# Kernel tuning notes

Hardware: AMD Instinct MI355X
Metric: run time of the kernel (lower is better)

Reference implementation:

```python
import jax, jax.numpy as jnp
import numpy as np

DESC_DIM = 128


def setup_inputs() -> dict:
    key = jax.random.key(0)
    # [B=1, desc_dim+1, H, W] dense Unet output: 128 descriptor channels + 1 heatmap channel
    features = jax.random.normal(key, (1, DESC_DIM + 1, 1024, 1024), dtype=jnp.float32)
    return {
        "features": features,
        "orig_w": 1024,
        "orig_h": 1024,
        "max_keypoints": 2048,
        "window": 5,
    }


def reference(features, orig_w, orig_h, max_keypoints, window):
    # DISK.detect + DISK.compute (inference path):
    # max-pool NMS on heatmap, keep positives inside original image bounds,
    # take top max_keypoints by score, gather + L2-normalize descriptors.
    D = features.shape[1] - 1
    heatmap = features[0, D]            # [H, W]
    desc = features[0, :D]              # [D, H, W]
    H, W = heatmap.shape

    # local-max NMS: equality with 5x5 max pool (ties measure-zero for float data)
    pooled = jax.lax.reduce_window(
        heatmap, -jnp.inf, jax.lax.max,
        window_dimensions=(window, window), window_strides=(1, 1), padding="SAME")
    ys = jnp.arange(H)[:, None]
    xs = jnp.arange(W)[None, :]
    in_bounds = (xs <= orig_w - 1) & (ys <= orig_h - 1)  # 'valid' filter in detect()
    mask = (heatmap == pooled) & (heatmap > 0.0) & in_bounds  # cutoff=0.0

    # replace nonzero + kthvalue + argsort with masked top-k (jit-friendly, same math)
    flat = jnp.where(mask, heatmap, -jnp.inf).reshape(-1)  # [H*W]
    scores, idx = jax.lax.top_k(flat, max_keypoints)       # [K], [K]
    y = idx // W
    x = idx % W
    keypoints = jnp.stack([x, y], axis=-1).astype(jnp.float32)  # [K, 2] (x, y)

    d = desc.reshape(D, -1)[:, idx].T                      # [K, D] gather
    d = d / jnp.maximum(jnp.linalg.norm(d, axis=-1, keepdims=True), 1e-12)  # F.normalize

    valid = jnp.isfinite(scores)  # padding indicator when fewer than K detections
    return keypoints, scores, d, valid
```

## Files before the change

kernel.cpp:

```cpp
#include <hip/hip_runtime.h>
#include <stdint.h>
#include <math.h>

#define WIDTH  1024
#define HEIGHT 1024
#define DDIM   128
#define TOPK   2048
#define CAP    131072
#define SELCAP 4096

#define HIST_OFF 64
#define KEYS_OFF (HIST_OFF + 65536 * 4)
#define SEL_OFF  (KEYS_OFF + CAP * 8)
#define SIDX_OFF (SEL_OFF + SELCAP * 8)

__global__ __launch_bounds__(1024) void find_candidates(
        const float* __restrict__ feat,
        const int* __restrict__ p_ow, const int* __restrict__ p_oh,
        unsigned int* __restrict__ hdr,
        unsigned int* __restrict__ hist,
        unsigned long long* __restrict__ keys) {
    const int x = threadIdx.x;
    const int y = blockIdx.x;
    const float* hm = feat + (size_t)DDIM * WIDTH * HEIGHT;

    __shared__ unsigned long long lkeys[256];
    __shared__ unsigned int lcnt, lbase;
    if (x == 0) lcnt = 0u;
    __syncthreads();

    float c = hm[y * WIDTH + x];
    if ((c > 0.0f) && (x <= p_ow[0] - 1) && (y <= p_oh[0] - 1)) {
        int xm2 = max(x - 2, 0), xm1 = max(x - 1, 0);
        int xp1 = min(x + 1, WIDTH - 1), xp2 = min(x + 2, WIDTH - 1);
        int ym2 = max(y - 2, 0), ym1 = max(y - 1, 0);
        int yp1 = min(y + 1, HEIGHT - 1), yp2 = min(y + 2, HEIGHT - 1);
        const float* r0 = hm + ym1 * WIDTH;
        const float* r1 = hm + y   * WIDTH;
        const float* r2 = hm + yp1 * WIDTH;
        float m = fmaxf(fmaxf(fmaxf(r0[xm1], r0[x]), fmaxf(r0[xp1], r1[xm1])),
                        fmaxf(fmaxf(r1[xp1], r2[xm1]), fmaxf(r2[x], r2[xp1])));
        if (m <= c) {
            const float* ra = hm + ym2 * WIDTH;
            const float* rb = hm + yp2 * WIDTH;
            float m2 = fmaxf(fmaxf(fmaxf(ra[xm2], ra[xm1]), fmaxf(ra[x], ra[xp1])), ra[xp2]);
            m2 = fmaxf(m2, fmaxf(fmaxf(rb[xm2], rb[xm1]), fmaxf(fmaxf(rb[x], rb[xp1]), rb[xp2])));
            m2 = fmaxf(m2, fmaxf(fmaxf(r0[xm2], r0[xp2]), fmaxf(r1[xm2], r1[xp2])));
            m2 = fmaxf(m2, fmaxf(r2[xm2], r2[xp2]));
            if (m2 <= c) {
                unsigned int idx = (unsigned int)(y * WIDTH + x);
                unsigned long long key =
                    ((unsigned long long)__float_as_uint(c) << 32) |
                    (unsigned long long)(~idx);
                unsigned int p = atomicAdd(&lcnt, 1u);
                if (p < 256u) lkeys[p] = key;
            }
        }
    }
    __syncthreads();
    if (x == 0) lbase = atomicAdd(&hdr[0], lcnt);
    __syncthreads();
    unsigned int n = lcnt < 256u ? lcnt : 256u;
    unsigned int base = lbase;
    for (unsigned int i = x; i < n; i += blockDim.x) {
        unsigned long long k = lkeys[i];
        if (base + i < CAP) keys[base + i] = k;
        atomicAdd(&hist[(unsigned int)(k >> 48)], 1u);
    }
}

__global__ __launch_bounds__(1024) void scan_hist(
        unsigned int* __restrict__ hdr,
        const unsigned int* __restrict__ hist) {
    __shared__ unsigned int part[1024];
    const int tid = threadIdx.x;
    const unsigned int base = (unsigned int)tid * 64u;
    unsigned int s = 0;
    #pragma unroll 8
    for (int j = 0; j < 64; ++j) s += hist[base + j];
    part[tid] = s;
    __syncthreads();
    for (int d = 1; d < 1024; d <<= 1) {
        unsigned int v = (tid + d < 1024) ? part[tid + d] : 0u;
        __syncthreads();
        part[tid] += v;
        __syncthreads();
    }
    unsigned int N = hdr[0]; if (N > CAP) N = CAP;
    unsigned int target = N < TOPK ? N : TOPK;
    if (tid == 0) { hdr[3] = target; if (target == 0) hdr[2] = 0u; }
    if (target == 0) return;
    unsigned int St = part[tid];
    unsigned int Sn = (tid < 1023) ? part[tid + 1] : 0u;
    if (St >= target && Sn < target) {
        unsigned int above = Sn;
        unsigned int B = base;
        for (int b = (int)base + 63; b >= (int)base; --b) {
            unsigned int h = hist[b];
            if (above + h >= target) { B = (unsigned int)b; break; }
            above += h;
        }
        hdr[2] = B;
    }
}

__global__ void filter_keys(unsigned int* __restrict__ hdr,
                            const unsigned long long* __restrict__ keys,
                            unsigned long long* __restrict__ sel) {
    unsigned int N = hdr[0]; if (N > CAP) N = CAP;
    unsigned long long B = (unsigned long long)hdr[2];
    unsigned int stride = gridDim.x * blockDim.x;
    for (unsigned int i = blockIdx.x * blockDim.x + threadIdx.x; i < N; i += stride) {
        unsigned long long k = keys[i];
        if ((k >> 48) >= B) {
            unsigned int p = atomicAdd(&hdr[1], 1u);
            if (p < SELCAP) sel[p] = k;
        }
    }
}

__global__ __launch_bounds__(1024) void sort_emit(
        const unsigned int* __restrict__ hdr,
        const unsigned long long* __restrict__ sel,
        float* __restrict__ out_kp, float* __restrict__ out_sc,
        float* __restrict__ out_vd, unsigned int* __restrict__ sidx) {
    __shared__ unsigned long long sk[SELCAP];
    const int tid = threadIdx.x;
    unsigned int M = hdr[1]; if (M > SELCAP) M = SELCAP;
    unsigned int KK = hdr[3];
    for (unsigned int i = tid; i < SELCAP; i += 1024) sk[i] = (i < M) ? sel[i] : 0ull;
    __syncthreads();
    for (unsigned int size = 2; size <= SELCAP; size <<= 1) {
        for (unsigned int str = size >> 1; str > 0; str >>= 1) {
            for (unsigned int i = tid; i < SELCAP; i += 1024) {
                unsigned int j = i ^ str;
                if (j > i) {
                    unsigned long long a = sk[i], b = sk[j];
                    bool desc = ((i & size) == 0);
                    if (desc ? (a < b) : (a > b)) { sk[i] = b; sk[j] = a; }
                }
            }
            __syncthreads();
        }
    }
    for (unsigned int r = tid; r < TOPK; r += 1024) {
        unsigned long long k = sk[r];
        bool live = (r < KK);
        unsigned int idx = ~(unsigned int)(k & 0xFFFFFFFFull);
        out_kp[2 * r + 0] = live ? (float)(idx & (WIDTH - 1)) : 0.0f;
        out_kp[2 * r + 1] = live ? (float)(idx >> 10) : 0.0f;
        out_sc[r] = live ? __uint_as_float((unsigned int)(k >> 32)) : -INFINITY;
        out_vd[r] = live ? 1.0f : 0.0f;
        sidx[r]   = live ? idx : 0u;
    }
}

__global__ __launch_bounds__(128) void gather_desc(
        const float* __restrict__ feat,
        const unsigned int* __restrict__ sidx,
        float* __restrict__ out_d) {
    int kp = blockIdx.x;
    int c  = threadIdx.x;
    unsigned int idx = sidx[kp];
    float v = feat[(size_t)c * (WIDTH * HEIGHT) + idx];
    float s = v * v;
    #pragma unroll
    for (int off = 32; off > 0; off >>= 1) s += __shfl_down(s, off, 64);
    __shared__ float sw[2];
    if ((c & 63) == 0) sw[c >> 6] = s;
    __syncthreads();
    float norm = fmaxf(sqrtf(sw[0] + sw[1]), 1e-12f);
    out_d[(size_t)kp * DDIM + c] = v / norm;
}

extern "C" void kernel_launch(void* const* d_in, const int* in_sizes, int n_in,
                              void* d_out, int out_size, void* d_ws, size_t ws_size,
                              hipStream_t stream) {
    const float* feat = (const float*)d_in[0];
    const int* p_ow = (const int*)d_in[1];
    const int* p_oh = (const int*)d_in[2];

    float* out = (float*)d_out;
    float* out_kp = out;
    float* out_sc = out + 2 * TOPK;
    float* out_d  = out + 3 * TOPK;
    float* out_vd = out + 3 * TOPK + TOPK * DDIM;

    unsigned int* hdr  = (unsigned int*)d_ws;
    unsigned int* hist = (unsigned int*)((char*)d_ws + HIST_OFF);
    unsigned long long* keys = (unsigned long long*)((char*)d_ws + KEYS_OFF);
    unsigned long long* sel  = (unsigned long long*)((char*)d_ws + SEL_OFF);
    unsigned int* sidx = (unsigned int*)((char*)d_ws + SIDX_OFF);

    hipMemsetAsync(d_ws, 0, KEYS_OFF, stream);

    find_candidates<<<HEIGHT, 1024, 0, stream>>>(feat, p_ow, p_oh, hdr, hist, keys);
    scan_hist<<<1, 1024, 0, stream>>>(hdr, hist);
    filter_keys<<<128, 256, 0, stream>>>(hdr, keys, sel);
    sort_emit<<<1, 1024, 0, stream>>>(hdr, sel, out_kp, out_sc, out_vd, sidx);
    gather_desc<<<TOPK, DDIM, 0, stream>>>(feat, sidx, out_d);
}
```

Baseline: 697.0 us.

## Fuse histogram scan, key filtering and sort into one kernel with two-level histogram

Replaces the separate scan, filter and sort kernels with a single block kernel that finds the threshold bin via a two-level 256x256 radix histogram, compacts candidate keys into shared memory using wave ballots, then bitonic sorts. This removes two kernel launches and a global selection buffer round trip. In exchange, the candidate kernel performs an extra global atomic per key and filtering is serialized onto one block.

```diff
diff --git a/kernel.cpp b/kernel.cpp
--- a/kernel.cpp
+++ b/kernel.cpp
@@ -10,9 +10,9 @@
 #define SELCAP 4096
 
 #define HIST_OFF 64
-#define KEYS_OFF (HIST_OFF + 65536 * 4)
-#define SEL_OFF  (KEYS_OFF + CAP * 8)
-#define SIDX_OFF (SEL_OFF + SELCAP * 8)
+#define HIST_N   (256 + 65536)
+#define KEYS_OFF (HIST_OFF + HIST_N * 4)
+#define SIDX_OFF (KEYS_OFF + CAP * 8)
 
 __global__ __launch_bounds__(1024) void find_candidates(
         const float* __restrict__ feat,
@@ -65,74 +65,85 @@
     for (unsigned int i = x; i < n; i += blockDim.x) {
         unsigned long long k = lkeys[i];
         if (base + i < CAP) keys[base + i] = k;
-        atomicAdd(&hist[(unsigned int)(k >> 48)], 1u);
-    }
-}
-
-__global__ __launch_bounds__(1024) void scan_hist(
-        unsigned int* __restrict__ hdr,
-        const unsigned int* __restrict__ hist) {
-    __shared__ unsigned int part[1024];
-    const int tid = threadIdx.x;
-    const unsigned int base = (unsigned int)tid * 64u;
-    unsigned int s = 0;
-    #pragma unroll 8
-    for (int j = 0; j < 64; ++j) s += hist[base + j];
-    part[tid] = s;
-    __syncthreads();
-    for (int d = 1; d < 1024; d <<= 1) {
-        unsigned int v = (tid + d < 1024) ? part[tid + d] : 0u;
-        __syncthreads();
-        part[tid] += v;
-        __syncthreads();
-    }
-    unsigned int N = hdr[0]; if (N > CAP) N = CAP;
-    unsigned int target = N < TOPK ? N : TOPK;
-    if (tid == 0) { hdr[3] = target; if (target == 0) hdr[2] = 0u; }
-    if (target == 0) return;
-    unsigned int St = part[tid];
-    unsigned int Sn = (tid < 1023) ? part[tid + 1] : 0u;
-    if (St >= target && Sn < target) {
-        unsigned int above = Sn;
-        unsigned int B = base;
-        for (int b = (int)base + 63; b >= (int)base; --b) {
-            unsigned int h = hist[b];
-            if (above + h >= target) { B = (unsigned int)b; break; }
-            above += h;
-        }
-        hdr[2] = B;
-    }
-}
-
-__global__ void filter_keys(unsigned int* __restrict__ hdr,
-                            const unsigned long long* __restrict__ keys,
-                            unsigned long long* __restrict__ sel) {
-    unsigned int N = hdr[0]; if (N > CAP) N = CAP;
-    unsigned long long B = (unsigned long long)hdr[2];
-    unsigned int stride = gridDim.x * blockDim.x;
-    for (unsigned int i = blockIdx.x * blockDim.x + threadIdx.x; i < N; i += stride) {
-        unsigned long long k = keys[i];
-        if ((k >> 48) >= B) {
-            unsigned int p = atomicAdd(&hdr[1], 1u);
-            if (p < SELCAP) sel[p] = k;
-        }
-    }
-}
-
-__global__ __launch_bounds__(1024) void sort_emit(
+        atomicAdd(&hist[(unsigned int)(k >> 56)], 1u);
+        atomicAdd(&hist[256u + (unsigned int)(k >> 48)], 1u);
+    }
+}
+
+__global__ __launch_bounds__(1024) void select_sort_emit(
         const unsigned int* __restrict__ hdr,
-        const unsigned long long* __restrict__ sel,
+        const unsigned int* __restrict__ hist,
+        const unsigned long long* __restrict__ keys,
         float* __restrict__ out_kp, float* __restrict__ out_sc,
         float* __restrict__ out_vd, unsigned int* __restrict__ sidx) {
     __shared__ unsigned long long sk[SELCAP];
+    __shared__ unsigned int scn[256];
+    __shared__ unsigned int sBc, sAc, sB, sCnt;
     const int tid = threadIdx.x;
-    unsigned int M = hdr[1]; if (M > SELCAP) M = SELCAP;
-    unsigned int KK = hdr[3];
-    for (unsigned int i = tid; i < SELCAP; i += 1024) sk[i] = (i < M) ? sel[i] : 0ull;
-    __syncthreads();
+    const int lane = tid & 63;
+
+    unsigned int N = hdr[0]; if (N > CAP) N = CAP;
+    unsigned int target = N < TOPK ? N : TOPK;
+
+    if (tid == 0) { sBc = 0u; sAc = 0u; sB = 0u; sCnt = 0u; }
+    if (tid < 256) scn[tid] = hist[tid];
+    __syncthreads();
+    for (int d = 1; d < 256; d <<= 1) {
+        unsigned int v = 0u;
+        if (tid < 256 && tid + d < 256) v = scn[tid + d];
+        __syncthreads();
+        if (tid < 256) scn[tid] += v;
+        __syncthreads();
+    }
+    if (tid < 256 && target > 0) {
+        unsigned int St = scn[tid];
+        unsigned int Sn = (tid < 255) ? scn[tid + 1] : 0u;
+        if (St >= target && Sn < target) { sBc = (unsigned int)tid; sAc = Sn; }
+    }
+    __syncthreads();
+    unsigned int bc = sBc, ac = sAc;
+    if (tid < 256) scn[tid] = hist[256u + bc * 256u + (unsigned int)tid];
+    __syncthreads();
+    for (int d = 1; d < 256; d <<= 1) {
+        unsigned int v = 0u;
+        if (tid < 256 && tid + d < 256) v = scn[tid + d];
+        __syncthreads();
+        if (tid < 256) scn[tid] += v;
+        __syncthreads();
+    }
+    if (tid < 256 && target > 0) {
+        unsigned int St = ac + scn[tid];
+        unsigned int Sn = ac + ((tid < 255) ? scn[tid + 1] : 0u);
+        if (St >= target && Sn < target) sB = (bc << 8) | (unsigned int)tid;
+    }
+    __syncthreads();
+    unsigned int B = sB;
+
+    if (target > 0) {
+        for (unsigned int i = tid; i < ((N + 1023u) & ~1023u); i += 1024u) {
+            unsigned long long k = (i < N) ? keys[i] : 0ull;
+            bool pred = (i < N) && ((unsigned int)(k >> 48) >= B);
+            unsigned long long mask = __ballot(pred);
+            if (mask) {
+                int leader = (int)(__ffsll((long long)mask) - 1);
+                unsigned int wbase = 0u;
+                if (lane == leader) wbase = atomicAdd(&sCnt, (unsigned int)__popcll(mask));
+                wbase = (unsigned int)__shfl((int)wbase, leader, 64);
+                if (pred) {
+                    unsigned int p = wbase + (unsigned int)__popcll(mask & ((1ull << lane) - 1ull));
+                    if (p < SELCAP) sk[p] = k;
+                }
+            }
+        }
+    }
+    __syncthreads();
+    unsigned int M = sCnt < SELCAP ? sCnt : SELCAP;
+    for (unsigned int i = M + tid; i < SELCAP; i += 1024u) sk[i] = 0ull;
+    __syncthreads();
+
     for (unsigned int size = 2; size <= SELCAP; size <<= 1) {
         for (unsigned int str = size >> 1; str > 0; str >>= 1) {
-            for (unsigned int i = tid; i < SELCAP; i += 1024) {
+            for (unsigned int i = tid; i < SELCAP; i += 1024u) {
                 unsigned int j = i ^ str;
                 if (j > i) {
                     unsigned long long a = sk[i], b = sk[j];
@@ -143,9 +154,10 @@
             __syncthreads();
         }
     }
-    for (unsigned int r = tid; r < TOPK; r += 1024) {
+
+    for (unsigned int r = tid; r < TOPK; r += 1024u) {
         unsigned long long k = sk[r];
-        bool live = (r < KK);
+        bool live = (r < target);
         unsigned int idx = ~(unsigned int)(k & 0xFFFFFFFFull);
         out_kp[2 * r + 0] = live ? (float)(idx & (WIDTH - 1)) : 0.0f;
         out_kp[2 * r + 1] = live ? (float)(idx >> 10) : 0.0f;
@@ -189,14 +201,12 @@
     unsigned int* hdr  = (unsigned int*)d_ws;
     unsigned int* hist = (unsigned int*)((char*)d_ws + HIST_OFF);
     unsigned long long* keys = (unsigned long long*)((char*)d_ws + KEYS_OFF);
-    unsigned long long* sel  = (unsigned long long*)((char*)d_ws + SEL_OFF);
     unsigned int* sidx = (unsigned int*)((char*)d_ws + SIDX_OFF);
 
     hipMemsetAsync(d_ws, 0, KEYS_OFF, stream);
 
     find_candidates<<<HEIGHT, 1024, 0, stream>>>(feat, p_ow, p_oh, hdr, hist, keys);
-    scan_hist<<<1, 1024, 0, stream>>>(hdr, hist);
-    filter_keys<<<128, 256, 0, stream>>>(hdr, keys, sel);
-    sort_emit<<<1, 1024, 0, stream>>>(hdr, sel, out_kp, out_sc, out_vd, sidx);
+    select_sort_emit<<<1, 1024, 0, stream>>>(hdr, hist, keys,
+                                             out_kp, out_sc, out_vd, sidx);
     gather_desc<<<TOPK, DDIM, 0, stream>>>(feat, sidx, out_d);
 }
```

Result: slower. 955.6 us (+37.1%).
